# Performance work log

Measured on AMD Instinct MI355X. Metric: run time of the kernel, lower is better.

Reference implementation:

```python
import jax, jax.numpy as jnp
import numpy as np

B, CH, N = 4, 128, 4096
PC = CH // 2  # pos channels = 64


def setup_inputs() -> dict:
    key = jax.random.key(0)
    ks = jax.random.split(key, 6)
    s_p = 1.0 / np.sqrt(PC)
    s_v = 1.0 / np.sqrt(CH)
    return {
        "pos_bot": jax.random.normal(ks[0], (B, PC, N), dtype=jnp.float32),
        "corr_feats": jax.random.normal(ks[1], (B, CH, N), dtype=jnp.float32),
        "Wp": jax.random.uniform(ks[2], (PC, PC), jnp.float32, -s_p, s_p),
        "bp": jax.random.uniform(ks[3], (PC,), jnp.float32, -s_p, s_p),
        "Wv": jax.random.uniform(ks[4], (CH, CH), jnp.float32, -s_v, s_v),
        "bv": jax.random.uniform(ks[5], (CH,), jnp.float32, -s_v, s_v),
        "beta": jnp.asarray([1.0], dtype=jnp.float32),
    }


def reference(pos_bot, corr_feats, Wp, bp, Wv, bv, beta):
    # 1x1 Conv1d == per-position matmul over channels
    pos = jnp.einsum("oc,bcn->bon", Wp, pos_bot) + bp[None, :, None]      # [B,64,N]
    value = jnp.einsum("oc,bcn->bon", Wv, corr_feats) + bv[None, :, None]  # [B,128,N]

    x = jnp.transpose(pos, (0, 2, 1))  # [B,N,64]
    # squared euclidean pairwise distance: ||xi||^2 + ||xj||^2 - 2 xi.xj
    sq = jnp.sum(x * x, axis=-1)  # [B,N]
    d2 = sq[:, :, None] + sq[:, None, :] - 2.0 * jnp.einsum("bnd,bmd->bnm", x, x)
    d2 = jnp.maximum(d2, 0.0)
    kernel = jnp.exp(-d2 * beta[0])  # [B,N,N] Gaussian RBF

    equation_F = jnp.transpose(value, (0, 2, 1))  # [B,N,128]
    return kernel, equation_F
```

## Files before the change

### kernel.cpp

```cpp
#include <hip/hip_runtime.h>
#include <hip/hip_bf16.h>

typedef _Float16 f16x8 __attribute__((ext_vector_type(8)));
typedef float    f32x4 __attribute__((ext_vector_type(4)));

constexpr int BB = 4;
constexpr int CH = 128;
constexpr int PC = 64;
constexpr int NN = 4096;

__global__ __launch_bounds__(256) void proj_kernel(
    const float* __restrict__ pos_bot,
    const float* __restrict__ corr,
    const float* __restrict__ Wp,
    const float* __restrict__ bp,
    const float* __restrict__ Wv,
    const float* __restrict__ bv,
    float*    __restrict__ eqF,
    _Float16* __restrict__ xbuf,
    float*    __restrict__ sq)
{
    const int tid  = threadIdx.x;
    const int wid  = tid >> 6;
    const int lane = tid & 63;
    const int l15  = lane & 15;
    const int lg   = lane >> 4;
    const int b    = blockIdx.y;
    const int nb   = blockIdx.x * 64 + wid * 16;
    const int n    = nb + l15;

    const f32x4 zero = {0.f, 0.f, 0.f, 0.f};

    f16x8 wf[4][2];
#pragma unroll
    for (int mt = 0; mt < 4; ++mt)
#pragma unroll
        for (int ks = 0; ks < 2; ++ks) {
            const float* wp = Wp + (mt * 16 + l15) * PC + ks * 32 + lg * 8;
            f32x4 w0 = *reinterpret_cast<const f32x4*>(wp);
            f32x4 w1 = *reinterpret_cast<const f32x4*>(wp + 4);
            f16x8 f;
#pragma unroll
            for (int e = 0; e < 4; ++e) { f[e] = (_Float16)w0[e]; f[e + 4] = (_Float16)w1[e]; }
            wf[mt][ks] = f;
        }

    f16x8 pb[2];
#pragma unroll
    for (int ks = 0; ks < 2; ++ks) {
        f16x8 f;
#pragma unroll
        for (int e = 0; e < 8; ++e) {
            const int c = ks * 32 + lg * 8 + e;
            f[e] = (_Float16)pos_bot[((size_t)(b * PC + c)) * NN + n];
        }
        pb[ks] = f;
    }

    f32x4 pacc[4] = {zero, zero, zero, zero};
#pragma unroll
    for (int ks = 0; ks < 2; ++ks)
#pragma unroll
        for (int mt = 0; mt < 4; ++mt)
            pacc[mt] = __builtin_amdgcn_mfma_f32_16x16x32_f16(wf[mt][ks], pb[ks], pacc[mt], 0, 0, 0);

    float sqp = 0.f;
#pragma unroll
    for (int mt = 0; mt < 4; ++mt)
#pragma unroll
        for (int r = 0; r < 4; ++r) {
            const int o = mt * 16 + lg * 4 + r;
            const float v = pacc[mt][r] + bp[o];
            const _Float16 h = (_Float16)v;
            xbuf[((size_t)(b * NN + n)) * PC + o] = h;
            const float hf = (float)h;
            sqp = fmaf(hf, hf, sqp);
        }
    sqp += __shfl_xor(sqp, 16);
    sqp += __shfl_xor(sqp, 32);
    if (lg == 0) sq[b * NN + n] = sqp;

    f16x8 cb[4];
#pragma unroll
    for (int ks = 0; ks < 4; ++ks) {
        f16x8 f;
#pragma unroll
        for (int e = 0; e < 8; ++e) {
            const int c = ks * 32 + lg * 8 + e;
            f[e] = (_Float16)corr[((size_t)(b * CH + c)) * NN + n];
        }
        cb[ks] = f;
    }

#pragma unroll
    for (int oh = 0; oh < 2; ++oh) {
        f16x8 wvf[4][4];
#pragma unroll
        for (int mt = 0; mt < 4; ++mt)
#pragma unroll
            for (int ks = 0; ks < 4; ++ks) {
                const float* wv = Wv + (oh * 64 + mt * 16 + l15) * CH + ks * 32 + lg * 8;
                f32x4 w0 = *reinterpret_cast<const f32x4*>(wv);
                f32x4 w1 = *reinterpret_cast<const f32x4*>(wv + 4);
                f16x8 f;
#pragma unroll
                for (int e = 0; e < 4; ++e) { f[e] = (_Float16)w0[e]; f[e + 4] = (_Float16)w1[e]; }
                wvf[mt][ks] = f;
            }

        f32x4 vacc[4] = {zero, zero, zero, zero};
#pragma unroll
        for (int ks = 0; ks < 4; ++ks)
#pragma unroll
            for (int mt = 0; mt < 4; ++mt)
                vacc[mt] = __builtin_amdgcn_mfma_f32_16x16x32_f16(wvf[mt][ks], cb[ks], vacc[mt], 0, 0, 0);

#pragma unroll
        for (int mt = 0; mt < 4; ++mt)
#pragma unroll
            for (int r = 0; r < 4; ++r) {
                const int o = oh * 64 + mt * 16 + lg * 4 + r;
                eqF[((size_t)(b * NN + n)) * CH + o] = vacc[mt][r] + bv[o];
            }
    }
}

__global__ __launch_bounds__(256) void gram_kernel(
    const _Float16* __restrict__ xbuf,
    const float*    __restrict__ sq,
    const float*    __restrict__ beta,
    float*          __restrict__ out)
{
    const int tid  = threadIdx.x;
    const int wid  = tid >> 6;
    const int lane = tid & 63;
    const int l15  = lane & 15;
    const int lg   = lane >> 4;
    const int wr   = wid >> 1;
    const int wc   = wid & 1;
    const int b    = blockIdx.z;
    const int ib   = blockIdx.x * 128 + wr * 64;
    const int jb   = blockIdx.y * 128 + wc * 64;

    const _Float16* xb = xbuf + (size_t)b * NN * PC;
    const f32x4 zero = {0.f, 0.f, 0.f, 0.f};

    f16x8 af[4][2], bf[4][2];
#pragma unroll
    for (int t = 0; t < 4; ++t)
#pragma unroll
        for (int ks = 0; ks < 2; ++ks) {
            af[t][ks] = *reinterpret_cast<const f16x8*>(
                xb + (size_t)(ib + t * 16 + l15) * PC + ks * 32 + lg * 8);
            bf[t][ks] = *reinterpret_cast<const f16x8*>(
                xb + (size_t)(jb + t * 16 + l15) * PC + ks * 32 + lg * 8);
        }

    f32x4 acc[4][4];
#pragma unroll
    for (int it = 0; it < 4; ++it)
#pragma unroll
        for (int jt = 0; jt < 4; ++jt) acc[it][jt] = zero;

#pragma unroll
    for (int ks = 0; ks < 2; ++ks)
#pragma unroll
        for (int it = 0; it < 4; ++it)
#pragma unroll
            for (int jt = 0; jt < 4; ++jt)
                acc[it][jt] = __builtin_amdgcn_mfma_f32_16x16x32_f16(
                    af[it][ks], bf[jt][ks], acc[it][jt], 0, 0, 0);

    const float* sqb = sq + (size_t)b * NN;
    float sqj[4];
#pragma unroll
    for (int jt = 0; jt < 4; ++jt) sqj[jt] = sqb[jb + jt * 16 + l15];

    const float bs = -beta[0] * 1.44269504088896f;

#pragma unroll
    for (int it = 0; it < 4; ++it) {
        float sqi[4];
#pragma unroll
        for (int r = 0; r < 4; ++r) sqi[r] = sqb[ib + it * 16 + lg * 4 + r];
#pragma unroll
        for (int jt = 0; jt < 4; ++jt) {
#pragma unroll
            for (int r = 0; r < 4; ++r) {
                float d2 = sqi[r] + sqj[jt] - 2.f * acc[it][jt][r];
                d2 = fmaxf(d2, 0.f);
                const float kv = __builtin_amdgcn_exp2f(bs * d2);
                const int i = ib + it * 16 + lg * 4 + r;
                const int j = jb + jt * 16 + l15;
                out[((size_t)(b * NN + i)) * NN + j] = kv;
            }
        }
    }
}

extern "C" void kernel_launch(void* const* d_in, const int* in_sizes, int n_in,
                              void* d_out, int out_size, void* d_ws, size_t ws_size,
                              hipStream_t stream) {
    const float* pos_bot = (const float*)d_in[0];
    const float* corr    = (const float*)d_in[1];
    const float* Wp      = (const float*)d_in[2];
    const float* bp      = (const float*)d_in[3];
    const float* Wv      = (const float*)d_in[4];
    const float* bv      = (const float*)d_in[5];
    const float* beta    = (const float*)d_in[6];

    float* out = (float*)d_out;
    float* eqF = out + (size_t)BB * NN * NN;

    _Float16* xbuf = (_Float16*)d_ws;
    float* sq = (float*)((char*)d_ws + (size_t)BB * NN * PC * sizeof(_Float16));

    proj_kernel<<<dim3(NN / 64, BB), 256, 0, stream>>>(
        pos_bot, corr, Wp, bp, Wv, bv, eqF, xbuf, sq);

    gram_kernel<<<dim3(NN / 128, NN / 128, BB), 256, 0, stream>>>(
        xbuf, sq, beta, out);
}
```

Baseline: 73.93 us.

## Split value projection into gram launch, vectorize output stores and spread pos projection

The value projection moves out of the serial pre-pass into extra blocks (z == BB) of the gram launch, so it overlaps with the RBF kernel computation. The pos projection is split over four waves per 16 columns, giving more blocks, and the squared-norm partial sums are combined in shared memory. The gram MFMA operands are swapped so each lane holds four consecutive j values, which allows 16-byte vectorized stores of the large N×N output. The exponent is also folded into a single fma with a clamp. The price is a heterogeneous grid and one barrier in the pos kernel.

```diff
diff --git a/kernel.cpp b/kernel.cpp
--- a/kernel.cpp
+++ b/kernel.cpp
@@ -2,6 +2,7 @@
 #include <hip/hip_bf16.h>
 
 typedef _Float16 f16x8 __attribute__((ext_vector_type(8)));
+typedef _Float16 f16x4 __attribute__((ext_vector_type(4)));
 typedef float    f32x4 __attribute__((ext_vector_type(4)));
 
 constexpr int BB = 4;
@@ -9,14 +10,10 @@
 constexpr int PC = 64;
 constexpr int NN = 4096;
 
-__global__ __launch_bounds__(256) void proj_kernel(
+__global__ __launch_bounds__(256) void proj_pos_kernel(
     const float* __restrict__ pos_bot,
-    const float* __restrict__ corr,
     const float* __restrict__ Wp,
     const float* __restrict__ bp,
-    const float* __restrict__ Wv,
-    const float* __restrict__ bv,
-    float*    __restrict__ eqF,
     _Float16* __restrict__ xbuf,
     float*    __restrict__ sq)
 {
@@ -26,121 +23,114 @@
     const int l15  = lane & 15;
     const int lg   = lane >> 4;
     const int b    = blockIdx.y;
-    const int nb   = blockIdx.x * 64 + wid * 16;
-    const int n    = nb + l15;
-
-    const f32x4 zero = {0.f, 0.f, 0.f, 0.f};
-
-    f16x8 wf[4][2];
-#pragma unroll
-    for (int mt = 0; mt < 4; ++mt)
-#pragma unroll
-        for (int ks = 0; ks < 2; ++ks) {
-            const float* wp = Wp + (mt * 16 + l15) * PC + ks * 32 + lg * 8;
-            f32x4 w0 = *reinterpret_cast<const f32x4*>(wp);
-            f32x4 w1 = *reinterpret_cast<const f32x4*>(wp + 4);
-            f16x8 f;
-#pragma unroll
-            for (int e = 0; e < 4; ++e) { f[e] = (_Float16)w0[e]; f[e + 4] = (_Float16)w1[e]; }
-            wf[mt][ks] = f;
-        }
-
-    f16x8 pb[2];
+    const int n    = blockIdx.x * 16 + l15;
+    const int mt   = wid;
+
+    f16x8 wf[2], pb[2];
 #pragma unroll
     for (int ks = 0; ks < 2; ++ks) {
+        const float* wp = Wp + (mt * 16 + l15) * PC + ks * 32 + lg * 8;
+        f32x4 w0 = *reinterpret_cast<const f32x4*>(wp);
+        f32x4 w1 = *reinterpret_cast<const f32x4*>(wp + 4);
         f16x8 f;
+#pragma unroll
+        for (int e = 0; e < 4; ++e) { f[e] = (_Float16)w0[e]; f[e + 4] = (_Float16)w1[e]; }
+        wf[ks] = f;
+        f16x8 g;
 #pragma unroll
         for (int e = 0; e < 8; ++e) {
             const int c = ks * 32 + lg * 8 + e;
-            f[e] = (_Float16)pos_bot[((size_t)(b * PC + c)) * NN + n];
-        }
-        pb[ks] = f;
-    }
-
-    f32x4 pacc[4] = {zero, zero, zero, zero};
-#pragma unroll
-    for (int ks = 0; ks < 2; ++ks)
-#pragma unroll
-        for (int mt = 0; mt < 4; ++mt)
-            pacc[mt] = __builtin_amdgcn_mfma_f32_16x16x32_f16(wf[mt][ks], pb[ks], pacc[mt], 0, 0, 0);
-
-    float sqp = 0.f;
-#pragma unroll
-    for (int mt = 0; mt < 4; ++mt)
-#pragma unroll
-        for (int r = 0; r < 4; ++r) {
-            const int o = mt * 16 + lg * 4 + r;
-            const float v = pacc[mt][r] + bp[o];
-            const _Float16 h = (_Float16)v;
-            xbuf[((size_t)(b * NN + n)) * PC + o] = h;
-            const float hf = (float)h;
-            sqp = fmaf(hf, hf, sqp);
-        }
-    sqp += __shfl_xor(sqp, 16);
-    sqp += __shfl_xor(sqp, 32);
-    if (lg == 0) sq[b * NN + n] = sqp;
-
-    f16x8 cb[4];
-#pragma unroll
-    for (int ks = 0; ks < 4; ++ks) {
-        f16x8 f;
-#pragma unroll
-        for (int e = 0; e < 8; ++e) {
-            const int c = ks * 32 + lg * 8 + e;
-            f[e] = (_Float16)corr[((size_t)(b * CH + c)) * NN + n];
-        }
-        cb[ks] = f;
-    }
-
-#pragma unroll
-    for (int oh = 0; oh < 2; ++oh) {
-        f16x8 wvf[4][4];
-#pragma unroll
-        for (int mt = 0; mt < 4; ++mt)
-#pragma unroll
-            for (int ks = 0; ks < 4; ++ks) {
-                const float* wv = Wv + (oh * 64 + mt * 16 + l15) * CH + ks * 32 + lg * 8;
-                f32x4 w0 = *reinterpret_cast<const f32x4*>(wv);
-                f32x4 w1 = *reinterpret_cast<const f32x4*>(wv + 4);
-                f16x8 f;
-#pragma unroll
-                for (int e = 0; e < 4; ++e) { f[e] = (_Float16)w0[e]; f[e + 4] = (_Float16)w1[e]; }
-                wvf[mt][ks] = f;
-            }
-
-        f32x4 vacc[4] = {zero, zero, zero, zero};
-#pragma unroll
-        for (int ks = 0; ks < 4; ++ks)
-#pragma unroll
-            for (int mt = 0; mt < 4; ++mt)
-                vacc[mt] = __builtin_amdgcn_mfma_f32_16x16x32_f16(wvf[mt][ks], cb[ks], vacc[mt], 0, 0, 0);
-
-#pragma unroll
-        for (int mt = 0; mt < 4; ++mt)
-#pragma unroll
-            for (int r = 0; r < 4; ++r) {
-                const int o = oh * 64 + mt * 16 + lg * 4 + r;
-                eqF[((size_t)(b * NN + n)) * CH + o] = vacc[mt][r] + bv[o];
-            }
-    }
+            g[e] = (_Float16)pos_bot[((size_t)(b * PC + c)) * NN + n];
+        }
+        pb[ks] = g;
+    }
+
+    f32x4 acc = {0.f, 0.f, 0.f, 0.f};
+    acc = __builtin_amdgcn_mfma_f32_16x16x32_f16(wf[0], pb[0], acc, 0, 0, 0);
+    acc = __builtin_amdgcn_mfma_f32_16x16x32_f16(wf[1], pb[1], acc, 0, 0, 0);
+
+    float partial = 0.f;
+    f16x4 h4;
+#pragma unroll
+    for (int r = 0; r < 4; ++r) {
+        const int o = mt * 16 + lg * 4 + r;
+        const float v = acc[r] + bp[o];
+        const _Float16 h = (_Float16)v;
+        h4[r] = h;
+        const float hf = (float)h;
+        partial = fmaf(hf, hf, partial);
+    }
+    *reinterpret_cast<f16x4*>(xbuf + ((size_t)(b * NN + n)) * PC + mt * 16 + lg * 4) = h4;
+
+    partial += __shfl_xor(partial, 16);
+    partial += __shfl_xor(partial, 32);
+    __shared__ float psum[4][16];
+    if (lane < 16) psum[wid][l15] = partial;
+    __syncthreads();
+    if (tid < 16)
+        sq[b * NN + blockIdx.x * 16 + tid] =
+            psum[0][tid] + psum[1][tid] + psum[2][tid] + psum[3][tid];
 }
 
 __global__ __launch_bounds__(256) void gram_kernel(
     const _Float16* __restrict__ xbuf,
     const float*    __restrict__ sq,
     const float*    __restrict__ beta,
-    float*          __restrict__ out)
+    float*          __restrict__ out,
+    const float*    __restrict__ corr,
+    const float*    __restrict__ Wv,
+    const float*    __restrict__ bv,
+    float*          __restrict__ eqF)
 {
     const int tid  = threadIdx.x;
     const int wid  = tid >> 6;
     const int lane = tid & 63;
     const int l15  = lane & 15;
     const int lg   = lane >> 4;
-    const int wr   = wid >> 1;
-    const int wc   = wid & 1;
-    const int b    = blockIdx.z;
-    const int ib   = blockIdx.x * 128 + wr * 64;
-    const int jb   = blockIdx.y * 128 + wc * 64;
+
+    if (blockIdx.z == BB) {
+        const int blk = blockIdx.y * 32 + blockIdx.x;
+        const int b   = blk >> 8;
+        const int n   = (blk & 255) * 16 + l15;
+
+        f16x8 cb[4];
+#pragma unroll
+        for (int ks = 0; ks < 4; ++ks) {
+            f16x8 g;
+#pragma unroll
+            for (int e = 0; e < 8; ++e) {
+                const int c = ks * 32 + lg * 8 + e;
+                g[e] = (_Float16)corr[((size_t)(b * CH + c)) * NN + n];
+            }
+            cb[ks] = g;
+        }
+#pragma unroll
+        for (int half = 0; half < 2; ++half) {
+            const int ot = wid + half * 4;
+            f32x4 acc = {0.f, 0.f, 0.f, 0.f};
+#pragma unroll
+            for (int ks = 0; ks < 4; ++ks) {
+                const float* wv = Wv + (ot * 16 + l15) * CH + ks * 32 + lg * 8;
+                f32x4 w0 = *reinterpret_cast<const f32x4*>(wv);
+                f32x4 w1 = *reinterpret_cast<const f32x4*>(wv + 4);
+                f16x8 f;
+#pragma unroll
+                for (int e = 0; e < 4; ++e) { f[e] = (_Float16)w0[e]; f[e + 4] = (_Float16)w1[e]; }
+                acc = __builtin_amdgcn_mfma_f32_16x16x32_f16(f, cb[ks], acc, 0, 0, 0);
+            }
+            f32x4 o4;
+#pragma unroll
+            for (int r = 0; r < 4; ++r) o4[r] = acc[r] + bv[ot * 16 + lg * 4 + r];
+            *reinterpret_cast<f32x4*>(eqF + ((size_t)(b * NN + n)) * CH + ot * 16 + lg * 4) = o4;
+        }
+        return;
+    }
+
+    const int wr = wid >> 1;
+    const int wc = wid & 1;
+    const int b  = blockIdx.z;
+    const int ib = blockIdx.x * 128 + wr * 64;
+    const int jb = blockIdx.y * 128 + wc * 64;
 
     const _Float16* xb = xbuf + (size_t)b * NN * PC;
     const f32x4 zero = {0.f, 0.f, 0.f, 0.f};
@@ -169,31 +159,34 @@
 #pragma unroll
             for (int jt = 0; jt < 4; ++jt)
                 acc[it][jt] = __builtin_amdgcn_mfma_f32_16x16x32_f16(
-                    af[it][ks], bf[jt][ks], acc[it][jt], 0, 0, 0);
+                    bf[jt][ks], af[it][ks], acc[it][jt], 0, 0, 0);
 
     const float* sqb = sq + (size_t)b * NN;
-    float sqj[4];
-#pragma unroll
-    for (int jt = 0; jt < 4; ++jt) sqj[jt] = sqb[jb + jt * 16 + l15];
-
-    const float bs = -beta[0] * 1.44269504088896f;
+    const float bs   = -beta[0] * 1.44269504088896f;
+    const float m2bs = -2.f * bs;
+
+    f32x4 tj[4];
+#pragma unroll
+    for (int jt = 0; jt < 4; ++jt) {
+        f32x4 s = *reinterpret_cast<const f32x4*>(sqb + jb + jt * 16 + lg * 4);
+        tj[jt] = s * bs;
+    }
 
 #pragma unroll
     for (int it = 0; it < 4; ++it) {
-        float sqi[4];
-#pragma unroll
-        for (int r = 0; r < 4; ++r) sqi[r] = sqb[ib + it * 16 + lg * 4 + r];
+        const int i   = ib + it * 16 + l15;
+        const float ti = bs * sqb[i];
+        float* orow = out + ((size_t)(b * NN + i)) * NN;
 #pragma unroll
         for (int jt = 0; jt < 4; ++jt) {
+            f32x4 v;
 #pragma unroll
             for (int r = 0; r < 4; ++r) {
-                float d2 = sqi[r] + sqj[jt] - 2.f * acc[it][jt][r];
-                d2 = fmaxf(d2, 0.f);
-                const float kv = __builtin_amdgcn_exp2f(bs * d2);
-                const int i = ib + it * 16 + lg * 4 + r;
-                const int j = jb + jt * 16 + l15;
-                out[((size_t)(b * NN + i)) * NN + j] = kv;
+                float arg = fmaf(m2bs, acc[it][jt][r], ti + tj[jt][r]);
+                arg = fminf(arg, 0.f);
+                v[r] = __builtin_amdgcn_exp2f(arg);
             }
+            *reinterpret_cast<f32x4*>(orow + jb + jt * 16 + lg * 4) = v;
         }
     }
 }
@@ -215,9 +208,8 @@
     _Float16* xbuf = (_Float16*)d_ws;
     float* sq = (float*)((char*)d_ws + (size_t)BB * NN * PC * sizeof(_Float16));
 
-    proj_kernel<<<dim3(NN / 64, BB), 256, 0, stream>>>(
-        pos_bot, corr, Wp, bp, Wv, bv, eqF, xbuf, sq);
-
-    gram_kernel<<<dim3(NN / 128, NN / 128, BB), 256, 0, stream>>>(
-        xbuf, sq, beta, out);
+    proj_pos_kernel<<<dim3(NN / 16, BB), 256, 0, stream>>>(pos_bot, Wp, bp, xbuf, sq);
+
+    gram_kernel<<<dim3(NN / 128, NN / 128, BB + 1), 256, 0, stream>>>(
+        xbuf, sq, beta, out, corr, Wv, bv, eqF);
 }
```

After: 79.95 us. 1.08x slower.
